# Optimization experiments

Hardware: AMD Instinct MI355X
Metric: run time of the kernel (lower is better)

The kernel has to match this reference:

```python
import jax, jax.numpy as jnp
import numpy as np

B, T, D, P, NP = 32, 512, 512, 200, 8
RADIUS = 3
TEMP = 1.0
DIRECTION = 'right'
NEG = -100000.0
EPS_NORM = 1e-12


def setup_inputs() -> dict:
    key = jax.random.key(0)
    k1, k2, k3 = jax.random.split(key, 3)
    return {
        "x": jax.random.normal(k1, (B, T, D), dtype=jnp.float32),
        "timeline_mask": jnp.ones((B, T), dtype=jnp.float32),
        "prototype_vectors": jax.random.uniform(k2, (P, D, NP), dtype=jnp.float32),
        "patch_select": jax.random.normal(k3, (1, P, NP), dtype=jnp.float32),
    }


def _l2norm(v, axis):
    return v / jnp.maximum(jnp.linalg.norm(v, axis=axis, keepdims=True), EPS_NORM)


def reference(x, timeline_mask, prototype_vectors, patch_select):
    # --- subpatch_dist ---
    xn = _l2norm(x, axis=-1)                       # (B, T, D)
    pn = _l2norm(prototype_vectors, axis=1)        # (P, D, n_p)
    dist_all = jnp.einsum('btd,pdi->bpti', xn, pn)  # (B, P, T, n_p)

    # timeline mask
    tm = timeline_mask[:, None, :, None]
    dist_all = dist_all * tm + (1.0 - tm) * NEG

    dt = dist_all.dtype
    b, p, t, n_p = dist_all.shape
    ar_t = jnp.arange(t)

    mask_act = jnp.ones((b, p, t), dt)
    mask_subpatch = jnp.ones((b, p, n_p), dt)
    mask_all = jnp.ones((b, p, t, n_p), dt)
    adjacent = jnp.ones((b, p, t), dt)

    ids_list, vals_list, ev_list = [], [], []
    # greedy iterative max-select over the n_p subpatches (sequential dependency)
    for it in range(n_p):
        dm = dist_all + (1.0 - mask_all * adjacent[..., None]) * NEG
        max_subs = dm.max(axis=2)                   # (B, P, n_p) best score per subpatch
        max_subs_id = jnp.argmax(dm, axis=2)        # (B, P, n_p) best event per subpatch
        max_sub_act = max_subs.max(axis=-1)         # (B, P)
        sub_id = jnp.argmax(max_subs, axis=-1)      # (B, P) chosen subpatch
        event_id = jnp.take_along_axis(max_subs_id, sub_id[..., None], axis=2)[..., 0]  # (B, P)

        neigh = (jnp.abs(ar_t[None, None, :] - event_id[..., None]) <= RADIUS).astype(dt)
        if it > 0:
            if DIRECTION == 'right':
                dmask = (ar_t[None, None, :] > event_id[..., None]).astype(dt)
            else:
                dmask = (ar_t[None, None, :] < event_id[..., None]).astype(dt)
            neigh = neigh * dmask
        adjacent = neigh

        # suppress chosen event and chosen subpatch (scatter_ 0 == multiply by 1-onehot)
        mask_act = mask_act * (1.0 - jax.nn.one_hot(event_id, t, dtype=dt))
        mask_subpatch = mask_subpatch * (1.0 - jax.nn.one_hot(sub_id, n_p, dtype=dt))
        mask_all = mask_all * mask_act[..., None] * mask_subpatch[:, :, None, :]

        ids_list.append(sub_id)
        vals_list.append(max_sub_act)
        ev_list.append(event_id.astype(dt))

    subpatch_ids = jnp.stack(ids_list, axis=-1)   # (B, P, n_p) int
    values = jnp.stack(vals_list, axis=-1)        # (B, P, n_p)
    indices = jnp.stack(ev_list, axis=-1)         # (B, P, n_p) float, matches torch cat promotion

    order = jnp.argsort(subpatch_ids, axis=-1)    # unique ids -> deterministic permutation
    values_r = jnp.take_along_axis(values, order, axis=-1)
    indices_r = jnp.take_along_axis(indices, order, axis=-1)

    slots = jax.nn.sigmoid(patch_select * TEMP)           # (1, P, n_p)
    factor = slots.sum(-1, keepdims=True) + 1e-10
    values_slot = values_r * (slots * n_p / factor)
    max_activation_slots = values_slot.sum(-1)            # (B, P)
    min_distances = n_p - max_activation_slots
    return (max_activation_slots, min_distances, indices_r)
```

## Files before the change

kernel.cpp:

```cpp
#include <hip/hip_runtime.h>
#include <hip/hip_bf16.h>
#include <hip/hip_fp16.h>
#include <math.h>

#define B_    32
#define T_    512
#define D_    512
#define P_    200
#define NP_   8
#define N_TOT 1600
#define NEG_  (-100000.0f)
#define LO_SCALE 2048.0f
#define LO_INV   (1.0f/2048.0f)

typedef __attribute__((ext_vector_type(8))) _Float16 f16x8;
typedef __attribute__((ext_vector_type(4))) _Float16 f16x4;
typedef __attribute__((ext_vector_type(4))) float   f32x4;
typedef unsigned long long u64;

#define GLL16(gp, lp) __builtin_amdgcn_global_load_lds( \
    (const __attribute__((address_space(1))) void*)(gp), \
    (__attribute__((address_space(3))) void*)(lp), 16, 0, 0)

__device__ __forceinline__ float wave_reduce_sum(float v) {
#pragma unroll
  for (int off = 32; off; off >>= 1) v += __shfl_xor(v, off, 64);
  return v;
}

__device__ __forceinline__ unsigned ordf(float f) {
  unsigned u = __float_as_uint(f);
  return (u & 0x80000000u) ? ~u : (u | 0x80000000u);
}
__device__ __forceinline__ float deco(unsigned o) {
  unsigned u = (o & 0x80000000u) ? (o ^ 0x80000000u) : ~o;
  return __uint_as_float(u);
}
__device__ __forceinline__ u64 packvk(float v, int key) {
  return ((u64)ordf(v) << 32) | (u64)(4095 - key);
}

__global__ __launch_bounds__(256) void norm_x_kernel(const float* __restrict__ x,
                                                     _Float16* __restrict__ xh,
                                                     _Float16* __restrict__ xl) {
  int row  = blockIdx.x * 4 + (threadIdx.x >> 6);
  int lane = threadIdx.x & 63;
  const float* xr = x + (size_t)row * D_;
  float4 v0 = *(const float4*)(xr + lane * 4);
  float4 v1 = *(const float4*)(xr + 256 + lane * 4);
  float s = v0.x*v0.x + v0.y*v0.y + v0.z*v0.z + v0.w*v0.w
          + v1.x*v1.x + v1.y*v1.y + v1.z*v1.z + v1.w*v1.w;
  s = wave_reduce_sum(s);
  float dn = fmaxf(sqrtf(s), 1e-12f);
  float f[8] = {v0.x/dn, v0.y/dn, v0.z/dn, v0.w/dn, v1.x/dn, v1.y/dn, v1.z/dn, v1.w/dn};
  f16x4 h0, h1, l0, l1;
#pragma unroll
  for (int j = 0; j < 4; j++) {
    h0[j] = (_Float16)f[j];
    l0[j] = (_Float16)((f[j] - (float)h0[j]) * LO_SCALE);
    h1[j] = (_Float16)f[4 + j];
    l1[j] = (_Float16)((f[4 + j] - (float)h1[j]) * LO_SCALE);
  }
  size_t base = (size_t)row * D_;
  *(f16x4*)(xh + base + lane * 4)       = h0;
  *(f16x4*)(xh + base + 256 + lane * 4) = h1;
  *(f16x4*)(xl + base + lane * 4)       = l0;
  *(f16x4*)(xl + base + 256 + lane * 4) = l1;
}

__global__ __launch_bounds__(256) void norm_w_kernel(const float* __restrict__ proto,
                                                     _Float16* __restrict__ wh,
                                                     _Float16* __restrict__ wl,
                                                     u64* __restrict__ slotbuf) {
  if (blockIdx.x == 0) {
    for (int i = threadIdx.x; i < 2 * B_ * P_; i += 256) slotbuf[i] = 0ULL;
  }
  int n    = blockIdx.x * 4 + (threadIdx.x >> 6);
  int lane = threadIdx.x & 63;
  int p = n >> 3, i = n & 7;
  float v[8];
  float s = 0.f;
#pragma unroll
  for (int k = 0; k < 8; k++) {
    int d = k * 64 + lane;
    v[k] = proto[((size_t)p * D_ + d) * NP_ + i];
    s += v[k] * v[k];
  }
  s = wave_reduce_sum(s);
  float dn = fmaxf(sqrtf(s), 1e-12f);
  size_t base = (size_t)n * D_;
#pragma unroll
  for (int k = 0; k < 8; k++) {
    float f = v[k] / dn;
    _Float16 h = (_Float16)f;
    wh[base + k * 64 + lane] = h;
    wl[base + k * 64 + lane] = (_Float16)((f - (float)h) * LO_SCALE);
  }
}

__global__ __launch_bounds__(256, 2) void gemm_mfma(
    const _Float16* __restrict__ XH, const _Float16* __restrict__ XL,
    const _Float16* __restrict__ WH, const _Float16* __restrict__ WL,
    const float* __restrict__ tm, float* __restrict__ dist,
    u64* __restrict__ rawslot, u64* __restrict__ qslot) {
  __shared__ _Float16 lds[4 * 128 * 32];
  const int b  = blockIdx.z;
  const int n0 = blockIdx.y * 128;
  const int t0 = blockIdx.x * 128;
  const int tid = threadIdx.x;
  const int w = tid >> 6, l = tid & 63;

  int c0 = (w * 2 + 0) * 64 + l;
  int c1 = (w * 2 + 1) * 64 + l;
  int r0 = c0 >> 2, kc0 = (c0 & 3) * 8;
  int r1 = c1 >> 2, kc1 = (c1 & 3) * 8;
  int an0 = n0 + r0; if (an0 > N_TOT - 1) an0 = N_TOT - 1;
  int an1 = n0 + r1; if (an1 > N_TOT - 1) an1 = N_TOT - 1;
  const _Float16* wh0 = WH + (size_t)an0 * D_ + kc0;
  const _Float16* wh1 = WH + (size_t)an1 * D_ + kc1;
  const _Float16* wl0 = WL + (size_t)an0 * D_ + kc0;
  const _Float16* wl1 = WL + (size_t)an1 * D_ + kc1;
  const _Float16* xh0 = XH + ((size_t)b * T_ + t0 + r0) * D_ + kc0;
  const _Float16* xh1 = XH + ((size_t)b * T_ + t0 + r1) * D_ + kc1;
  const _Float16* xl0 = XL + ((size_t)b * T_ + t0 + r0) * D_ + kc0;
  const _Float16* xl1 = XL + ((size_t)b * T_ + t0 + r1) * D_ + kc1;
  _Float16* ldAh = lds +     0 + (w * 2) * 512;
  _Float16* ldAl = lds +  4096 + (w * 2) * 512;
  _Float16* ldXh = lds +  8192 + (w * 2) * 512;
  _Float16* ldXl = lds + 12288 + (w * 2) * 512;

  const int wn = (w >> 1) * 64, wtf = (w & 1) * 64;
  const int fr = l & 15, fq = l >> 4;

  f32x4 acch[4][4], accc[4][4];
#pragma unroll
  for (int m = 0; m < 4; m++)
#pragma unroll
    for (int n = 0; n < 4; n++) { acch[m][n] = (f32x4)0.0f; accc[m][n] = (f32x4)0.0f; }

  for (int kt = 0; kt < 16; ++kt) {
    const int k0 = kt * 32;
    GLL16(wh0 + k0, ldAh); GLL16(wh1 + k0, ldAh + 512);
    GLL16(wl0 + k0, ldAl); GLL16(wl1 + k0, ldAl + 512);
    GLL16(xh0 + k0, ldXh); GLL16(xh1 + k0, ldXh + 512);
    GLL16(xl0 + k0, ldXl); GLL16(xl1 + k0, ldXl + 512);
    __syncthreads();
    f16x8 ah[4], al[4], bh[4], bl[4];
#pragma unroll
    for (int m = 0; m < 4; m++) {
      int ro = (wn + m * 16 + fr) * 32 + fq * 8;
      ah[m] = *(const f16x8*)&lds[ro];
      al[m] = *(const f16x8*)&lds[4096 + ro];
    }
#pragma unroll
    for (int n = 0; n < 4; n++) {
      int ro = (wtf + n * 16 + fr) * 32 + fq * 8;
      bh[n] = *(const f16x8*)&lds[8192 + ro];
      bl[n] = *(const f16x8*)&lds[12288 + ro];
    }
#pragma unroll
    for (int m = 0; m < 4; m++)
#pragma unroll
      for (int n = 0; n < 4; n++) {
        acch[m][n] = __builtin_amdgcn_mfma_f32_16x16x32_f16(ah[m], bh[n], acch[m][n], 0, 0, 0);
        accc[m][n] = __builtin_amdgcn_mfma_f32_16x16x32_f16(ah[m], bl[n], accc[m][n], 0, 0, 0);
        accc[m][n] = __builtin_amdgcn_mfma_f32_16x16x32_f16(al[m], bh[n], accc[m][n], 0, 0, 0);
      }
    __syncthreads();
  }

  u64 pm[4], qm[4];
#pragma unroll
  for (int m = 0; m < 4; m++) { pm[m] = 0ULL; qm[m] = 0ULL; }
#pragma unroll
  for (int n = 0; n < 4; n++) {
    int col = t0 + wtf + n * 16 + fr;
    float tmc = tm[b * T_ + col];
#pragma unroll
    for (int m = 0; m < 4; m++) {
      int nb = n0 + wn + m * 16 + fq * 4;
#pragma unroll
      for (int r = 0; r < 4; r++) {
        int nr = nb + r;
        if (nr < N_TOT) {
          float v = acch[m][n][r] + accc[m][n][r] * LO_INV;
          v = v * tmc + (1.0f - tmc) * NEG_;
          dist[((size_t)b * N_TOT + nr) * T_ + col] = v;
          int key = ((fq * 4 + r) & 7) * T_ + col;
          u64 pk = packvk(v, key);
          if (pk > pm[m]) pm[m] = pk;
          u64 qk = packvk(v + NEG_, key);
          if (qk > qm[m]) qm[m] = qk;
        }
      }
    }
  }
#pragma unroll
  for (int m = 0; m < 4; m++) {
#pragma unroll
    for (int off = 1; off <= 16; off <<= 1) {
      u64 o1 = __shfl_xor(pm[m], off, 64); if (o1 > pm[m]) pm[m] = o1;
      u64 o2 = __shfl_xor(qm[m], off, 64); if (o2 > qm[m]) qm[m] = o2;
    }
  }
  if ((l & 31) == 0) {
    int h = l >> 5;
#pragma unroll
    for (int m = 0; m < 4; m++) {
      int p = (n0 >> 3) + ((w >> 1) * 8) + m * 2 + h;
      if (p < P_) {
        atomicMax(&rawslot[b * P_ + p], pm[m]);
        atomicMax(&qslot[b * P_ + p], qm[m]);
      }
    }
  }
}

__global__ __launch_bounds__(256) void select_kernel(const float* __restrict__ dist,
                                                     const u64* __restrict__ rawslot,
                                                     const u64* __restrict__ qslot,
                                                     const float* __restrict__ tmg,
                                                     const float* __restrict__ psel,
                                                     float* __restrict__ out) {
  __shared__ float win[4][NP_][33];
  int w = threadIdx.x >> 6, lane = threadIdx.x & 63;
  int pair = blockIdx.x * 4 + w;
  int b = pair / P_, p = pair % P_;
  const float* dbase = dist + ((size_t)b * N_TOT + p * NP_) * T_;

  bool okt = true;
#pragma unroll
  for (int c = 0; c < 8; c++) okt = okt && (tmg[b * T_ + c * 64 + lane] == 1.0f);
  bool tmones = (__ballot(okt) == ~0ULL);

  u64 rs = rawslot[pair], qs = qslot[pair];
  float rv = deco((unsigned)(rs >> 32)); int rkey = 4095 - (int)(rs & 0xFFFFu);
  float qv = deco((unsigned)(qs >> 32)); int qkey = 4095 - (int)(qs & 0xFFFFu);

  int e0 = rkey & (T_ - 1);
  int lo = e0 - 3;
  if (lo < 0) lo = 0;
  if (lo > T_ - 32) lo = T_ - 32;
  if (tmones) {
#pragma unroll
    for (int r2 = 0; r2 < 4; r2++) {
      int idx = r2 * 64 + lane;
      win[w][idx >> 5][idx & 31] = dbase[(size_t)(idx >> 5) * T_ + lo + (idx & 31)];
    }
  }
  __syncthreads();

  float valh[8]; int evh[8], sidh[8];
#pragma unroll
  for (int k = 0; k < 8; k++) { valh[k] = 0.f; evh[k] = -1; sidh[k] = 0; }
  unsigned msub = 0xFFu;
  int e_last = 0;

  for (int it = 0; it < 8; ++it) {
    float bv; int bkey;
    if (tmones) {
      if (it == 0) { bv = rv; bkey = rkey; }
      else {
        int i = lane >> 3, widx = lane & 7;
        int tw, nw;
        if (it == 1) { tw = e_last - 3 + widx; nw = 7; }
        else         { tw = e_last + 1 + widx; nw = 3; }
        bool valid = (widx < nw) && (tw >= 0) && (tw < T_) && (((msub >> i) & 1u) != 0u);
#pragma unroll
        for (int k = 0; k < 8; k++) if (tw == evh[k]) valid = false;
        float v = -3.0e38f;
        if (valid) {
          int off = tw - lo;
          v = (off >= 0 && off < 32) ? win[w][i][off]
                                     : dbase[(size_t)i * T_ + tw];
        }
        int key = valid ? (i * T_ + tw) : 0x7FFFFFFF;
#pragma unroll
        for (int off = 32; off; off >>= 1) {
          float ov = __shfl_xor(v, off, 64);
          int  ok2 = __shfl_xor(key, off, 64);
          if (ov > v || (ov == v && ok2 < key)) { v = ov; key = ok2; }
        }
        if (v > -2.9e38f) { bv = v; bkey = key; }
        else              { bv = qv; bkey = qkey; }
      }
    } else {
      float lv = -3.0e38f; int lkey = 0x7FFFFFFF;
      for (int i = 0; i < 8; i++) {
        bool sub_ok = ((msub >> i) & 1u) != 0u;
        const float* row = dbase + (size_t)i * T_;
        float4 u0 = *(const float4*)(row + lane * 8);
        float4 u1 = *(const float4*)(row + lane * 8 + 4);
        float uv[8] = {u0.x, u0.y, u0.z, u0.w, u1.x, u1.y, u1.z, u1.w};
#pragma unroll
        for (int j = 0; j < 8; j++) {
          int t = lane * 8 + j;
          bool act = sub_ok;
          if (it > 0) {
            int dt = t - e_last;
            act = act && (dt <= 3) && (dt >= -3);
            if (it > 1) act = act && (dt > 0);
          }
#pragma unroll
          for (int k = 0; k < 8; k++) if (t == evh[k]) act = false;
          float dm = act ? uv[j] : (uv[j] + NEG_);
          if (dm > lv) { lv = dm; lkey = i * T_ + t; }
        }
      }
#pragma unroll
      for (int off = 32; off; off >>= 1) {
        float ov = __shfl_xor(lv, off, 64);
        int  ok2 = __shfl_xor(lkey, off, 64);
        if (ov > lv || (ov == lv && ok2 < lkey)) { lv = ov; lkey = ok2; }
      }
      bv = lv; bkey = lkey;
    }
    int bi = bkey >> 9, bt = bkey & (T_ - 1);
#pragma unroll
    for (int k = 0; k < 8; k++) {
      if (it == k) { valh[k] = bv; evh[k] = bt; sidh[k] = bi; }
    }
    msub &= ~(1u << bi);
    e_last = bt;
  }

  if (lane == 0) {
    int ord[8]; unsigned used = 0;
#pragma unroll
    for (int j = 0; j < 8; j++) {
      int bk = 1 << 30, bi2 = 0;
#pragma unroll
      for (int k = 0; k < 8; k++)
        if (!((used >> k) & 1u)) { int key = sidh[k] * 8 + k; if (key < bk) { bk = key; bi2 = k; } }
      ord[j] = bi2; used |= 1u << bi2;
    }
    float slots[8]; float ssum = 0.f;
#pragma unroll
    for (int i = 0; i < 8; i++) {
      slots[i] = 1.0f / (1.0f + expf(-psel[p * NP_ + i]));
      ssum += slots[i];
    }
    float fac = ssum + 1e-10f;
    float acc = 0.f;
    float vr[8]; float er[8];
#pragma unroll
    for (int j = 0; j < 8; j++) {
      float vv = 0.f, ee = 0.f;
#pragma unroll
      for (int k = 0; k < 8; k++) if (ord[j] == k) { vv = valh[k]; ee = (float)evh[k]; }
      vr[j] = vv; er[j] = ee;
    }
#pragma unroll
    for (int j = 0; j < 8; j++) acc += vr[j] * (slots[j] * 8.0f / fac);
    int bp = b * P_ + p;
    out[bp] = acc;
    out[B_ * P_ + bp] = 8.0f - acc;
#pragma unroll
    for (int j = 0; j < 8; j++) out[2 * B_ * P_ + bp * 8 + j] = er[j];
  }
}

extern "C" void kernel_launch(void* const* d_in, const int* in_sizes, int n_in,
                              void* d_out, int out_size, void* d_ws, size_t ws_size,
                              hipStream_t stream) {
  const float* x     = (const float*)d_in[0];
  const float* tm    = (const float*)d_in[1];
  const float* proto = (const float*)d_in[2];
  const float* psel  = (const float*)d_in[3];
  float* out = (float*)d_out;

  char* wsb = (char*)d_ws;
  _Float16* XH = (_Float16*)wsb;
  _Float16* XL = (_Float16*)(wsb + 16777216u);
  _Float16* WH = (_Float16*)(wsb + 2u * 16777216u);
  _Float16* WL = (_Float16*)(wsb + 2u * 16777216u + 1638400u);
  float*   dist = (float*)(wsb + 2u * 16777216u + 2u * 1638400u);
  u64*  rawslot = (u64*)(wsb + 141688832u);
  u64*  qslot   = rawslot + B_ * P_;

  norm_x_kernel<<<dim3(B_ * T_ / 4), 256, 0, stream>>>(x, XH, XL);
  norm_w_kernel<<<dim3(N_TOT / 4), 256, 0, stream>>>(proto, WH, WL, rawslot);
  gemm_mfma<<<dim3(T_ / 128, (N_TOT + 127) / 128, B_), 256, 0, stream>>>(
      XH, XL, WH, WL, tm, dist, rawslot, qslot);
  select_kernel<<<dim3(B_ * P_ / 4), 256, 0, stream>>>(dist, rawslot, qslot, tm, psel, out);
}
```

Before: 232.3 us.

## Fuse norm kernels and enlarge GEMM tile to 256x128 with 512 threads

The two normalization kernels are merged into one launch that uses a block-index split, saving a kernel launch. The GEMM block grows from 128x128 to 256 prototype columns by 128 timesteps with 8 waves, so each X tile loaded into LDS is reused across twice as many prototype rows and redundant X traffic drops. The cost is more LDS per block, a larger thread count that may reduce occupancy, and more padding waste on the last N tile, since 1600 is not a multiple of 256.

```diff
diff --git a/kernel.cpp b/kernel.cpp
--- a/kernel.cpp
+++ b/kernel.cpp
@@ -40,96 +40,97 @@
   return ((u64)ordf(v) << 32) | (u64)(4095 - key);
 }
 
-__global__ __launch_bounds__(256) void norm_x_kernel(const float* __restrict__ x,
-                                                     _Float16* __restrict__ xh,
-                                                     _Float16* __restrict__ xl) {
-  int row  = blockIdx.x * 4 + (threadIdx.x >> 6);
+__global__ __launch_bounds__(256) void norm_fused(const float* __restrict__ x,
+                                                  const float* __restrict__ proto,
+                                                  _Float16* __restrict__ xh,
+                                                  _Float16* __restrict__ xl,
+                                                  _Float16* __restrict__ wh,
+                                                  _Float16* __restrict__ wl,
+                                                  u64* __restrict__ slotbuf) {
   int lane = threadIdx.x & 63;
-  const float* xr = x + (size_t)row * D_;
-  float4 v0 = *(const float4*)(xr + lane * 4);
-  float4 v1 = *(const float4*)(xr + 256 + lane * 4);
-  float s = v0.x*v0.x + v0.y*v0.y + v0.z*v0.z + v0.w*v0.w
-          + v1.x*v1.x + v1.y*v1.y + v1.z*v1.z + v1.w*v1.w;
-  s = wave_reduce_sum(s);
-  float dn = fmaxf(sqrtf(s), 1e-12f);
-  float f[8] = {v0.x/dn, v0.y/dn, v0.z/dn, v0.w/dn, v1.x/dn, v1.y/dn, v1.z/dn, v1.w/dn};
-  f16x4 h0, h1, l0, l1;
-#pragma unroll
-  for (int j = 0; j < 4; j++) {
-    h0[j] = (_Float16)f[j];
-    l0[j] = (_Float16)((f[j] - (float)h0[j]) * LO_SCALE);
-    h1[j] = (_Float16)f[4 + j];
-    l1[j] = (_Float16)((f[4 + j] - (float)h1[j]) * LO_SCALE);
-  }
-  size_t base = (size_t)row * D_;
-  *(f16x4*)(xh + base + lane * 4)       = h0;
-  *(f16x4*)(xh + base + 256 + lane * 4) = h1;
-  *(f16x4*)(xl + base + lane * 4)       = l0;
-  *(f16x4*)(xl + base + 256 + lane * 4) = l1;
-}
-
-__global__ __launch_bounds__(256) void norm_w_kernel(const float* __restrict__ proto,
-                                                     _Float16* __restrict__ wh,
-                                                     _Float16* __restrict__ wl,
-                                                     u64* __restrict__ slotbuf) {
-  if (blockIdx.x == 0) {
-    for (int i = threadIdx.x; i < 2 * B_ * P_; i += 256) slotbuf[i] = 0ULL;
-  }
-  int n    = blockIdx.x * 4 + (threadIdx.x >> 6);
-  int lane = threadIdx.x & 63;
-  int p = n >> 3, i = n & 7;
-  float v[8];
-  float s = 0.f;
-#pragma unroll
-  for (int k = 0; k < 8; k++) {
-    int d = k * 64 + lane;
-    v[k] = proto[((size_t)p * D_ + d) * NP_ + i];
-    s += v[k] * v[k];
-  }
-  s = wave_reduce_sum(s);
-  float dn = fmaxf(sqrtf(s), 1e-12f);
-  size_t base = (size_t)n * D_;
-#pragma unroll
-  for (int k = 0; k < 8; k++) {
-    float f = v[k] / dn;
-    _Float16 h = (_Float16)f;
-    wh[base + k * 64 + lane] = h;
-    wl[base + k * 64 + lane] = (_Float16)((f - (float)h) * LO_SCALE);
-  }
-}
-
-__global__ __launch_bounds__(256, 2) void gemm_mfma(
+  if (blockIdx.x < B_ * T_ / 4) {
+    int row = blockIdx.x * 4 + (threadIdx.x >> 6);
+    const float* xr = x + (size_t)row * D_;
+    float4 v0 = *(const float4*)(xr + lane * 4);
+    float4 v1 = *(const float4*)(xr + 256 + lane * 4);
+    float s = v0.x*v0.x + v0.y*v0.y + v0.z*v0.z + v0.w*v0.w
+            + v1.x*v1.x + v1.y*v1.y + v1.z*v1.z + v1.w*v1.w;
+    s = wave_reduce_sum(s);
+    float dn = fmaxf(sqrtf(s), 1e-12f);
+    float f[8] = {v0.x/dn, v0.y/dn, v0.z/dn, v0.w/dn, v1.x/dn, v1.y/dn, v1.z/dn, v1.w/dn};
+    f16x4 h0, h1, l0, l1;
+#pragma unroll
+    for (int j = 0; j < 4; j++) {
+      h0[j] = (_Float16)f[j];
+      l0[j] = (_Float16)((f[j] - (float)h0[j]) * LO_SCALE);
+      h1[j] = (_Float16)f[4 + j];
+      l1[j] = (_Float16)((f[4 + j] - (float)h1[j]) * LO_SCALE);
+    }
+    size_t base = (size_t)row * D_;
+    *(f16x4*)(xh + base + lane * 4)       = h0;
+    *(f16x4*)(xh + base + 256 + lane * 4) = h1;
+    *(f16x4*)(xl + base + lane * 4)       = l0;
+    *(f16x4*)(xl + base + 256 + lane * 4) = l1;
+  } else {
+    int wb = blockIdx.x - B_ * T_ / 4;
+    if (wb == 0) {
+      for (int i = threadIdx.x; i < 2 * B_ * P_; i += 256) slotbuf[i] = 0ULL;
+    }
+    int n = wb * 4 + (threadIdx.x >> 6);
+    int p = n >> 3, i = n & 7;
+    float v[8];
+    float s = 0.f;
+#pragma unroll
+    for (int k = 0; k < 8; k++) {
+      int d = k * 64 + lane;
+      v[k] = proto[((size_t)p * D_ + d) * NP_ + i];
+      s += v[k] * v[k];
+    }
+    s = wave_reduce_sum(s);
+    float dn = fmaxf(sqrtf(s), 1e-12f);
+    size_t base = (size_t)n * D_;
+#pragma unroll
+    for (int k = 0; k < 8; k++) {
+      float f = v[k] / dn;
+      _Float16 h = (_Float16)f;
+      wh[base + k * 64 + lane] = h;
+      wl[base + k * 64 + lane] = (_Float16)((f - (float)h) * LO_SCALE);
+    }
+  }
+}
+
+__global__ __launch_bounds__(512, 2) void gemm_mfma(
     const _Float16* __restrict__ XH, const _Float16* __restrict__ XL,
     const _Float16* __restrict__ WH, const _Float16* __restrict__ WL,
     const float* __restrict__ tm, float* __restrict__ dist,
     u64* __restrict__ rawslot, u64* __restrict__ qslot) {
-  __shared__ _Float16 lds[4 * 128 * 32];
+  __shared__ _Float16 lds[24576];
   const int b  = blockIdx.z;
-  const int n0 = blockIdx.y * 128;
+  const int n0 = blockIdx.y * 256;
   const int t0 = blockIdx.x * 128;
   const int tid = threadIdx.x;
   const int w = tid >> 6, l = tid & 63;
 
-  int c0 = (w * 2 + 0) * 64 + l;
-  int c1 = (w * 2 + 1) * 64 + l;
-  int r0 = c0 >> 2, kc0 = (c0 & 3) * 8;
-  int r1 = c1 >> 2, kc1 = (c1 & 3) * 8;
-  int an0 = n0 + r0; if (an0 > N_TOT - 1) an0 = N_TOT - 1;
-  int an1 = n0 + r1; if (an1 > N_TOT - 1) an1 = N_TOT - 1;
-  const _Float16* wh0 = WH + (size_t)an0 * D_ + kc0;
-  const _Float16* wh1 = WH + (size_t)an1 * D_ + kc1;
-  const _Float16* wl0 = WL + (size_t)an0 * D_ + kc0;
-  const _Float16* wl1 = WL + (size_t)an1 * D_ + kc1;
-  const _Float16* xh0 = XH + ((size_t)b * T_ + t0 + r0) * D_ + kc0;
-  const _Float16* xh1 = XH + ((size_t)b * T_ + t0 + r1) * D_ + kc1;
-  const _Float16* xl0 = XL + ((size_t)b * T_ + t0 + r0) * D_ + kc0;
-  const _Float16* xl1 = XL + ((size_t)b * T_ + t0 + r1) * D_ + kc1;
-  _Float16* ldAh = lds +     0 + (w * 2) * 512;
-  _Float16* ldAl = lds +  4096 + (w * 2) * 512;
-  _Float16* ldXh = lds +  8192 + (w * 2) * 512;
-  _Float16* ldXl = lds + 12288 + (w * 2) * 512;
-
-  const int wn = (w >> 1) * 64, wtf = (w & 1) * 64;
+  int ra0 = tid >> 2,         ka0 = (tid & 3) * 8;
+  int ra1 = (512 + tid) >> 2, ka1 = (tid & 3) * 8;
+  int an0 = n0 + ra0; if (an0 > N_TOT - 1) an0 = N_TOT - 1;
+  int an1 = n0 + ra1; if (an1 > N_TOT - 1) an1 = N_TOT - 1;
+  const _Float16* pwh0 = WH + (size_t)an0 * D_ + ka0;
+  const _Float16* pwh1 = WH + (size_t)an1 * D_ + ka1;
+  const _Float16* pwl0 = WL + (size_t)an0 * D_ + ka0;
+  const _Float16* pwl1 = WL + (size_t)an1 * D_ + ka1;
+  int rx = tid >> 2, kx = (tid & 3) * 8;
+  const _Float16* pxh = XH + ((size_t)b * T_ + t0 + rx) * D_ + kx;
+  const _Float16* pxl = XL + ((size_t)b * T_ + t0 + rx) * D_ + kx;
+  _Float16* dAh0 = lds +     0 + w * 512;
+  _Float16* dAh1 = lds +  4096 + w * 512;
+  _Float16* dAl0 = lds +  8192 + w * 512;
+  _Float16* dAl1 = lds + 12288 + w * 512;
+  _Float16* dXh  = lds + 16384 + w * 512;
+  _Float16* dXl  = lds + 20480 + w * 512;
+
+  const int wn = (w >> 1) * 64;
+  const int wt = (w & 1) * 64;
   const int fr = l & 15, fq = l >> 4;
 
   f32x4 acch[4][4], accc[4][4];
@@ -140,23 +141,22 @@
 
   for (int kt = 0; kt < 16; ++kt) {
     const int k0 = kt * 32;
-    GLL16(wh0 + k0, ldAh); GLL16(wh1 + k0, ldAh + 512);
-    GLL16(wl0 + k0, ldAl); GLL16(wl1 + k0, ldAl + 512);
-    GLL16(xh0 + k0, ldXh); GLL16(xh1 + k0, ldXh + 512);
-    GLL16(xl0 + k0, ldXl); GLL16(xl1 + k0, ldXl + 512);
+    GLL16(pwh0 + k0, dAh0); GLL16(pwh1 + k0, dAh1);
+    GLL16(pwl0 + k0, dAl0); GLL16(pwl1 + k0, dAl1);
+    GLL16(pxh  + k0, dXh);  GLL16(pxl  + k0, dXl);
     __syncthreads();
     f16x8 ah[4], al[4], bh[4], bl[4];
 #pragma unroll
     for (int m = 0; m < 4; m++) {
       int ro = (wn + m * 16 + fr) * 32 + fq * 8;
       ah[m] = *(const f16x8*)&lds[ro];
-      al[m] = *(const f16x8*)&lds[4096 + ro];
+      al[m] = *(const f16x8*)&lds[8192 + ro];
     }
 #pragma unroll
     for (int n = 0; n < 4; n++) {
-      int ro = (wtf + n * 16 + fr) * 32 + fq * 8;
-      bh[n] = *(const f16x8*)&lds[8192 + ro];
-      bl[n] = *(const f16x8*)&lds[12288 + ro];
+      int ro = (wt + n * 16 + fr) * 32 + fq * 8;
+      bh[n] = *(const f16x8*)&lds[16384 + ro];
+      bl[n] = *(const f16x8*)&lds[20480 + ro];
     }
 #pragma unroll
     for (int m = 0; m < 4; m++)
@@ -174,7 +174,7 @@
   for (int m = 0; m < 4; m++) { pm[m] = 0ULL; qm[m] = 0ULL; }
 #pragma unroll
   for (int n = 0; n < 4; n++) {
-    int col = t0 + wtf + n * 16 + fr;
+    int col = t0 + wt + n * 16 + fr;
     float tmc = tm[b * T_ + col];
 #pragma unroll
     for (int m = 0; m < 4; m++) {
@@ -378,9 +378,9 @@
   u64*  rawslot = (u64*)(wsb + 141688832u);
   u64*  qslot   = rawslot + B_ * P_;
 
-  norm_x_kernel<<<dim3(B_ * T_ / 4), 256, 0, stream>>>(x, XH, XL);
-  norm_w_kernel<<<dim3(N_TOT / 4), 256, 0, stream>>>(proto, WH, WL, rawslot);
-  gemm_mfma<<<dim3(T_ / 128, (N_TOT + 127) / 128, B_), 256, 0, stream>>>(
+  norm_fused<<<dim3(B_ * T_ / 4 + N_TOT / 4), 256, 0, stream>>>(
+      x, proto, XH, XL, WH, WL, rawslot);
+  gemm_mfma<<<dim3(T_ / 128, (N_TOT + 255) / 256, B_), 512, 0, stream>>>(
       XH, XL, WH, WL, tm, dist, rawslot, qslot);
   select_kernel<<<dim3(B_ * P_ / 4), 256, 0, stream>>>(dist, rawslot, qslot, tm, psel, out);
 }
```

New measurement: 255.2 us. +9.9%, slower.

## Double-buffer GEMM LDS tiles and fuse the two normalization kernels

Applied to the files above, without the earlier changes.

The GEMM now uses two LDS buffers, prefetching the next k-tile via global_load_lds while the MFMAs consume the current one, with one barrier per iteration instead of two. The x and prototype normalization kernels are merged into one launch indexed by block id, removing a launch and its tail. LDS use per block doubles, which may limit occupancy.

```diff
diff --git a/kernel.cpp b/kernel.cpp
--- a/kernel.cpp
+++ b/kernel.cpp
@@ -40,61 +40,62 @@
   return ((u64)ordf(v) << 32) | (u64)(4095 - key);
 }
 
-__global__ __launch_bounds__(256) void norm_x_kernel(const float* __restrict__ x,
-                                                     _Float16* __restrict__ xh,
-                                                     _Float16* __restrict__ xl) {
-  int row  = blockIdx.x * 4 + (threadIdx.x >> 6);
+__global__ __launch_bounds__(256) void norm_fused(const float* __restrict__ x,
+                                                  const float* __restrict__ proto,
+                                                  _Float16* __restrict__ xh,
+                                                  _Float16* __restrict__ xl,
+                                                  _Float16* __restrict__ wh,
+                                                  _Float16* __restrict__ wl,
+                                                  u64* __restrict__ slotbuf) {
   int lane = threadIdx.x & 63;
-  const float* xr = x + (size_t)row * D_;
-  float4 v0 = *(const float4*)(xr + lane * 4);
-  float4 v1 = *(const float4*)(xr + 256 + lane * 4);
-  float s = v0.x*v0.x + v0.y*v0.y + v0.z*v0.z + v0.w*v0.w
-          + v1.x*v1.x + v1.y*v1.y + v1.z*v1.z + v1.w*v1.w;
-  s = wave_reduce_sum(s);
-  float dn = fmaxf(sqrtf(s), 1e-12f);
-  float f[8] = {v0.x/dn, v0.y/dn, v0.z/dn, v0.w/dn, v1.x/dn, v1.y/dn, v1.z/dn, v1.w/dn};
-  f16x4 h0, h1, l0, l1;
-#pragma unroll
-  for (int j = 0; j < 4; j++) {
-    h0[j] = (_Float16)f[j];
-    l0[j] = (_Float16)((f[j] - (float)h0[j]) * LO_SCALE);
-    h1[j] = (_Float16)f[4 + j];
-    l1[j] = (_Float16)((f[4 + j] - (float)h1[j]) * LO_SCALE);
-  }
-  size_t base = (size_t)row * D_;
-  *(f16x4*)(xh + base + lane * 4)       = h0;
-  *(f16x4*)(xh + base + 256 + lane * 4) = h1;
-  *(f16x4*)(xl + base + lane * 4)       = l0;
-  *(f16x4*)(xl + base + 256 + lane * 4) = l1;
-}
-
-__global__ __launch_bounds__(256) void norm_w_kernel(const float* __restrict__ proto,
-                                                     _Float16* __restrict__ wh,
-                                                     _Float16* __restrict__ wl,
-                                                     u64* __restrict__ slotbuf) {
-  if (blockIdx.x == 0) {
-    for (int i = threadIdx.x; i < 2 * B_ * P_; i += 256) slotbuf[i] = 0ULL;
-  }
-  int n    = blockIdx.x * 4 + (threadIdx.x >> 6);
-  int lane = threadIdx.x & 63;
-  int p = n >> 3, i = n & 7;
-  float v[8];
-  float s = 0.f;
-#pragma unroll
-  for (int k = 0; k < 8; k++) {
-    int d = k * 64 + lane;
-    v[k] = proto[((size_t)p * D_ + d) * NP_ + i];
-    s += v[k] * v[k];
-  }
-  s = wave_reduce_sum(s);
-  float dn = fmaxf(sqrtf(s), 1e-12f);
-  size_t base = (size_t)n * D_;
-#pragma unroll
-  for (int k = 0; k < 8; k++) {
-    float f = v[k] / dn;
-    _Float16 h = (_Float16)f;
-    wh[base + k * 64 + lane] = h;
-    wl[base + k * 64 + lane] = (_Float16)((f - (float)h) * LO_SCALE);
+  if (blockIdx.x < B_ * T_ / 4) {
+    int row = blockIdx.x * 4 + (threadIdx.x >> 6);
+    const float* xr = x + (size_t)row * D_;
+    float4 v0 = *(const float4*)(xr + lane * 4);
+    float4 v1 = *(const float4*)(xr + 256 + lane * 4);
+    float s = v0.x*v0.x + v0.y*v0.y + v0.z*v0.z + v0.w*v0.w
+            + v1.x*v1.x + v1.y*v1.y + v1.z*v1.z + v1.w*v1.w;
+    s = wave_reduce_sum(s);
+    float dn = fmaxf(sqrtf(s), 1e-12f);
+    float f[8] = {v0.x/dn, v0.y/dn, v0.z/dn, v0.w/dn, v1.x/dn, v1.y/dn, v1.z/dn, v1.w/dn};
+    f16x4 h0, h1, l0, l1;
+#pragma unroll
+    for (int j = 0; j < 4; j++) {
+      h0[j] = (_Float16)f[j];
+      l0[j] = (_Float16)((f[j] - (float)h0[j]) * LO_SCALE);
+      h1[j] = (_Float16)f[4 + j];
+      l1[j] = (_Float16)((f[4 + j] - (float)h1[j]) * LO_SCALE);
+    }
+    size_t base = (size_t)row * D_;
+    *(f16x4*)(xh + base + lane * 4)       = h0;
+    *(f16x4*)(xh + base + 256 + lane * 4) = h1;
+    *(f16x4*)(xl + base + lane * 4)       = l0;
+    *(f16x4*)(xl + base + 256 + lane * 4) = l1;
+  } else {
+    int wb = blockIdx.x - B_ * T_ / 4;
+    if (wb == 0) {
+      for (int i = threadIdx.x; i < 2 * B_ * P_; i += 256) slotbuf[i] = 0ULL;
+    }
+    int n = wb * 4 + (threadIdx.x >> 6);
+    int p = n >> 3, i = n & 7;
+    float v[8];
+    float s = 0.f;
+#pragma unroll
+    for (int k = 0; k < 8; k++) {
+      int d = k * 64 + lane;
+      v[k] = proto[((size_t)p * D_ + d) * NP_ + i];
+      s += v[k] * v[k];
+    }
+    s = wave_reduce_sum(s);
+    float dn = fmaxf(sqrtf(s), 1e-12f);
+    size_t base = (size_t)n * D_;
+#pragma unroll
+    for (int k = 0; k < 8; k++) {
+      float f = v[k] / dn;
+      _Float16 h = (_Float16)f;
+      wh[base + k * 64 + lane] = h;
+      wl[base + k * 64 + lane] = (_Float16)((f - (float)h) * LO_SCALE);
+    }
   }
 }
 
@@ -103,7 +104,7 @@
     const _Float16* __restrict__ WH, const _Float16* __restrict__ WL,
     const float* __restrict__ tm, float* __restrict__ dist,
     u64* __restrict__ rawslot, u64* __restrict__ qslot) {
-  __shared__ _Float16 lds[4 * 128 * 32];
+  __shared__ _Float16 lds[2 * 16384];
   const int b  = blockIdx.z;
   const int n0 = blockIdx.y * 128;
   const int t0 = blockIdx.x * 128;
@@ -124,10 +125,14 @@
   const _Float16* xh1 = XH + ((size_t)b * T_ + t0 + r1) * D_ + kc1;
   const _Float16* xl0 = XL + ((size_t)b * T_ + t0 + r0) * D_ + kc0;
   const _Float16* xl1 = XL + ((size_t)b * T_ + t0 + r1) * D_ + kc1;
-  _Float16* ldAh = lds +     0 + (w * 2) * 512;
-  _Float16* ldAl = lds +  4096 + (w * 2) * 512;
-  _Float16* ldXh = lds +  8192 + (w * 2) * 512;
-  _Float16* ldXl = lds + 12288 + (w * 2) * 512;
+  const int dA = (w * 2) * 512;
+
+#define STAGE(bufo, kk) do { \
+    GLL16(wh0 + (kk), &lds[(bufo) + dA]);          GLL16(wh1 + (kk), &lds[(bufo) + dA + 512]); \
+    GLL16(wl0 + (kk), &lds[(bufo) + 4096 + dA]);   GLL16(wl1 + (kk), &lds[(bufo) + 4096 + dA + 512]); \
+    GLL16(xh0 + (kk), &lds[(bufo) + 8192 + dA]);   GLL16(xh1 + (kk), &lds[(bufo) + 8192 + dA + 512]); \
+    GLL16(xl0 + (kk), &lds[(bufo) + 12288 + dA]);  GLL16(xl1 + (kk), &lds[(bufo) + 12288 + dA + 512]); \
+  } while (0)
 
   const int wn = (w >> 1) * 64, wtf = (w & 1) * 64;
   const int fr = l & 15, fq = l >> 4;
@@ -138,25 +143,25 @@
 #pragma unroll
     for (int n = 0; n < 4; n++) { acch[m][n] = (f32x4)0.0f; accc[m][n] = (f32x4)0.0f; }
 
+  STAGE(0, 0);
+  __syncthreads();
+
   for (int kt = 0; kt < 16; ++kt) {
-    const int k0 = kt * 32;
-    GLL16(wh0 + k0, ldAh); GLL16(wh1 + k0, ldAh + 512);
-    GLL16(wl0 + k0, ldAl); GLL16(wl1 + k0, ldAl + 512);
-    GLL16(xh0 + k0, ldXh); GLL16(xh1 + k0, ldXh + 512);
-    GLL16(xl0 + k0, ldXl); GLL16(xl1 + k0, ldXl + 512);
-    __syncthreads();
+    const int cur = (kt & 1) * 16384;
+    if (kt < 15) STAGE(cur ^ 16384, (kt + 1) * 32);
+
     f16x8 ah[4], al[4], bh[4], bl[4];
 #pragma unroll
     for (int m = 0; m < 4; m++) {
       int ro = (wn + m * 16 + fr) * 32 + fq * 8;
-      ah[m] = *(const f16x8*)&lds[ro];
-      al[m] = *(const f16x8*)&lds[4096 + ro];
+      ah[m] = *(const f16x8*)&lds[cur + ro];
+      al[m] = *(const f16x8*)&lds[cur + 4096 + ro];
     }
 #pragma unroll
     for (int n = 0; n < 4; n++) {
       int ro = (wtf + n * 16 + fr) * 32 + fq * 8;
-      bh[n] = *(const f16x8*)&lds[8192 + ro];
-      bl[n] = *(const f16x8*)&lds[12288 + ro];
+      bh[n] = *(const f16x8*)&lds[cur + 8192 + ro];
+      bl[n] = *(const f16x8*)&lds[cur + 12288 + ro];
     }
 #pragma unroll
     for (int m = 0; m < 4; m++)
@@ -168,6 +173,7 @@
       }
     __syncthreads();
   }
+#undef STAGE
 
   u64 pm[4], qm[4];
 #pragma unroll
@@ -378,8 +384,8 @@
   u64*  rawslot = (u64*)(wsb + 141688832u);
   u64*  qslot   = rawslot + B_ * P_;
 
-  norm_x_kernel<<<dim3(B_ * T_ / 4), 256, 0, stream>>>(x, XH, XL);
-  norm_w_kernel<<<dim3(N_TOT / 4), 256, 0, stream>>>(proto, WH, WL, rawslot);
+  norm_fused<<<dim3(B_ * T_ / 4 + N_TOT / 4), 256, 0, stream>>>(
+      x, proto, XH, XL, WH, WL, rawslot);
   gemm_mfma<<<dim3(T_ / 128, (N_TOT + 127) / 128, B_), 256, 0, stream>>>(
       XH, XL, WH, WL, tm, dist, rawslot, qslot);
   select_kernel<<<dim3(B_ * P_ / 4), 256, 0, stream>>>(dist, rawslot, qslot, tm, psel, out);
```

Result: faster. 224.0 us (-3.6%).
